# Optimization experiments

Hardware: AMD Instinct MI355X
Metric: run time of the kernel (lower is better)

The kernel has to match this reference:

```python
import jax, jax.numpy as jnp
import numpy as np

EPS = 1e-10

def setup_inputs() -> dict:
    key = jax.random.key(0)
    k0, k1, k2, k3, k4, k5 = jax.random.split(key, 6)
    B, S, V, C, D = 256, 20, 20000, 20, 64
    support_set_images = jax.random.uniform(k0, (B, S, V), dtype=jnp.float32)
    support_set_y_one_hot = jax.nn.one_hot(jax.random.randint(k1, (B, S), 0, C), C, dtype=jnp.float32)
    target_image = jax.random.uniform(k2, (B, V), dtype=jnp.float32)
    target_y = jax.random.randint(k3, (B,), 0, C)
    W = jax.random.normal(k4, (D, V), dtype=jnp.float32) * (1.0 / np.sqrt(V).astype(np.float32))
    b = jax.random.normal(k5, (D,), dtype=jnp.float32) * 0.01
    return dict(support_set_images=support_set_images,
                support_set_y_one_hot=support_set_y_one_hot,
                target_image=target_image, target_y=target_y, W=W, b=b)


def reference(support_set_images, support_set_y_one_hot, target_image, target_y, W, b):
    # SentenceEncoder (Linear vocab->64), applied to each support item and the target.
    sup = jnp.einsum('bsv,dv->bsd', support_set_images, W) + b        # [B,S,64]
    tgt = target_image @ W.T + b                                      # [B,64]

    # DistanceNetwork: dot(target, support) * rsqrt(clamp(||support||^2, eps))
    # (only the support vector's magnitude is normalized -- faithful to source).
    mag = jax.lax.rsqrt(jnp.clip(jnp.sum(sup * sup, axis=-1), EPS, None))  # [B,S]
    dots = jnp.einsum('bsd,bd->bs', sup, tgt)                              # [B,S]
    similarities = dots * mag                                              # [B,S]

    # AttentionalClassify: softmax over support, weighted combine of labels.
    attn = jax.nn.softmax(similarities, axis=-1)                           # [B,S]
    preds = jnp.einsum('bs,bsc->bc', attn, support_set_y_one_hot)          # [B,C]

    indices = jnp.argmax(preds, axis=1)
    accuracy = jnp.mean((indices == target_y).astype(jnp.float32))
    # F.cross_entropy applies log_softmax to preds (even though preds are already pdfs).
    logp = jax.nn.log_softmax(preds, axis=-1)
    crossentropy_loss = -jnp.mean(jnp.take_along_axis(logp, target_y[:, None], axis=1))
    return accuracy, crossentropy_loss
```

## Files before the change

kernel.cpp:

```cpp
#include <hip/hip_runtime.h>
#include <hip/hip_bf16.h>
#include <math.h>

#define B_  256
#define S_  20
#define V_  20000
#define C_  20
#define D_  64
#define MTOT (B_*S_ + B_)
#define KSPLIT 25
#define NK32 625
#define NKC  25

typedef __bf16 bf16x8 __attribute__((ext_vector_type(8)));
typedef float  f32x4  __attribute__((ext_vector_type(4)));

__device__ __forceinline__ void split8(const float4 a, const float4 b,
                                       uint4& hi, uint4& lo) {
    const float f[8] = {a.x, a.y, a.z, a.w, b.x, b.y, b.z, b.w};
    unsigned int h[8]; float r[8];
#pragma unroll
    for (int j = 0; j < 8; ++j) {
        const unsigned int u = __float_as_uint(f[j]);
        h[j] = u & 0xFFFF0000u;
        r[j] = f[j] - __uint_as_float(h[j]);
    }
    hi.x = (h[0] >> 16) | h[1];
    hi.y = (h[2] >> 16) | h[3];
    hi.z = (h[4] >> 16) | h[5];
    hi.w = (h[6] >> 16) | h[7];
    lo.x = (__float_as_uint(r[0]) >> 16) | (__float_as_uint(r[1]) & 0xFFFF0000u);
    lo.y = (__float_as_uint(r[2]) >> 16) | (__float_as_uint(r[3]) & 0xFFFF0000u);
    lo.z = (__float_as_uint(r[4]) >> 16) | (__float_as_uint(r[5]) & 0xFFFF0000u);
    lo.w = (__float_as_uint(r[6]) >> 16) | (__float_as_uint(r[7]) & 0xFFFF0000u);
}

__global__ __launch_bounds__(256)
void wconv_kernel(const float* __restrict__ W,
                  uint4* __restrict__ Wfh, uint4* __restrict__ Wfl) {
    const int g    = blockIdx.x * 256 + threadIdx.x;
    const int lane = g & 63;
    const int tt   = (g >> 6) & 3;
    const int c    = g >> 8;
    const int ln = lane & 15, qd = lane >> 4;
    const float* src = W + (size_t)(16 * tt + ln) * V_ + c * 32 + qd * 8;
    const float4 a = *(const float4*)src;
    const float4 b = *(const float4*)(src + 4);
    uint4 h, l; split8(a, b, h, l);
    Wfh[g] = h; Wfl[g] = l;
}

__global__ __launch_bounds__(256, 2)
void gemm3_kernel(const float* __restrict__ sup,
                  const float* __restrict__ tgtim,
                  const uint4* __restrict__ Wfh,
                  const uint4* __restrict__ Wfl,
                  float* __restrict__ Ep) {
    const int bmx = blockIdx.x;
    const int bk  = blockIdx.y;
    const int t = threadIdx.x;
    const int w = t >> 6, lane = t & 63;
    const int ln = lane & 15, qd = lane >> 4;
    const int mrow0 = bmx * 256 + w * 64;

    const float* xbase = (mrow0 < B_*S_)
        ? (sup   + (size_t)mrow0 * V_)
        : (tgtim + (size_t)(mrow0 - B_*S_) * V_);
    const float* xr0 = xbase + (size_t)ln * V_ + qd * 8;
    const float* xr1 = xr0 + (size_t)16 * V_;
    const float* xr2 = xr1 + (size_t)16 * V_;
    const float* xr3 = xr2 + (size_t)16 * V_;
    const uint4* wbh = Wfh + lane;
    const uint4* wbl = Wfl + lane;
    const int c0 = bk * NKC;

    f32x4 acc[4][4];
#pragma unroll
    for (int i = 0; i < 4; ++i)
#pragma unroll
        for (int j = 0; j < 4; ++j) acc[i][j] = (f32x4){0.f, 0.f, 0.f, 0.f};

    float4 aA[4][2], aB[4][2];
    uint4 whA[4], wlA[4], whB[4], wlB[4];

#define LDA(buf, c) do {                                                      \
    const size_t off_ = (size_t)(c) * 32;                                     \
    buf[0][0] = *(const float4*)(xr0 + off_);                                 \
    buf[0][1] = *(const float4*)(xr0 + off_ + 4);                             \
    buf[1][0] = *(const float4*)(xr1 + off_);                                 \
    buf[1][1] = *(const float4*)(xr1 + off_ + 4);                             \
    buf[2][0] = *(const float4*)(xr2 + off_);                                 \
    buf[2][1] = *(const float4*)(xr2 + off_ + 4);                             \
    buf[3][0] = *(const float4*)(xr3 + off_);                                 \
    buf[3][1] = *(const float4*)(xr3 + off_ + 4);                             \
} while (0)

#define LDW(bh_, bl_, c) do {                                                 \
    const uint4* ph_ = wbh + (size_t)(c) * 256;                               \
    const uint4* pl_ = wbl + (size_t)(c) * 256;                               \
    _Pragma("unroll")                                                         \
    for (int tt = 0; tt < 4; ++tt) { bh_[tt] = ph_[tt*64]; bl_[tt] = pl_[tt*64]; } \
} while (0)

#define STEP(abuf, bh_, bl_) do {                                             \
    _Pragma("unroll")                                                         \
    for (int af = 0; af < 4; ++af) {                                          \
        uint4 hu_, lu_; split8(abuf[af][0], abuf[af][1], hu_, lu_);           \
        const bf16x8 ah_ = *(const bf16x8*)&hu_;                              \
        const bf16x8 al_ = *(const bf16x8*)&lu_;                              \
        _Pragma("unroll")                                                     \
        for (int tt = 0; tt < 4; ++tt) {                                      \
            const bf16x8 bh2_ = *(const bf16x8*)&bh_[tt];                     \
            const bf16x8 bl2_ = *(const bf16x8*)&bl_[tt];                     \
            acc[af][tt] = __builtin_amdgcn_mfma_f32_16x16x32_bf16(ah_, bh2_, acc[af][tt], 0, 0, 0); \
            acc[af][tt] = __builtin_amdgcn_mfma_f32_16x16x32_bf16(ah_, bl2_, acc[af][tt], 0, 0, 0); \
            acc[af][tt] = __builtin_amdgcn_mfma_f32_16x16x32_bf16(al_, bh2_, acc[af][tt], 0, 0, 0); \
        }                                                                     \
    }                                                                         \
} while (0)

    LDA(aA, c0); LDW(whA, wlA, c0);
#pragma unroll 1
    for (int ii = 0; ii < (NKC - 1) / 2; ++ii) {
        const int c1 = c0 + 2 * ii + 1;
        LDA(aB, c1); LDW(whB, wlB, c1);
        STEP(aA, whA, wlA);
        const int c2 = c0 + 2 * ii + 2;
        LDA(aA, c2); LDW(whA, wlA, c2);
        STEP(aB, whB, wlB);
    }
    STEP(aA, whA, wlA);

#undef LDA
#undef LDW
#undef STEP

    float* dst = Ep + ((size_t)bk * MTOT + mrow0 + qd * 4) * D_ + ln;
#pragma unroll
    for (int af = 0; af < 4; ++af)
#pragma unroll
        for (int tt = 0; tt < 4; ++tt)
#pragma unroll
            for (int r = 0; r < 4; ++r)
                dst[(size_t)(af * 16 + r) * D_ + 16 * tt] = acc[af][tt][r];
}

__global__ __launch_bounds__(256)
void reduce_kernel(float* __restrict__ Ep) {
    const size_t i = (size_t)blockIdx.x * 256 + threadIdx.x;
    const size_t stride = (size_t)MTOT * D_;
    float4 s = *(const float4*)(Ep + i * 4);
#pragma unroll
    for (int p = 1; p < KSPLIT; ++p) {
        const float4 v = *(const float4*)(Ep + p * stride + i * 4);
        s.x += v.x; s.y += v.y; s.z += v.z; s.w += v.w;
    }
    *(float4*)(Ep + i * 4) = s;
}

__global__ __launch_bounds__(64)
void phase2_kernel(const float* __restrict__ E0,
                   const float* __restrict__ bias,
                   const float* __restrict__ onehot,
                   const int*   __restrict__ ty_,
                   float* __restrict__ res) {
    const int b = blockIdx.x;
    const int d = threadIdx.x;
    const float bv = bias[d];

    float supv[S_];
#pragma unroll
    for (int s = 0; s < S_; ++s)
        supv[s] = E0[((size_t)b * S_ + s) * D_ + d] + bv;
    float tg = E0[((size_t)(B_ * S_) + b) * D_ + d] + bv;

    float sims[S_];
#pragma unroll
    for (int s = 0; s < S_; ++s) {
        float q = supv[s] * supv[s];
        float r = supv[s] * tg;
#pragma unroll
        for (int off = 32; off; off >>= 1) {
            q += __shfl_xor(q, off);
            r += __shfl_xor(r, off);
        }
        sims[s] = r * rsqrtf(fmaxf(q, 1e-10f));
    }

    float mx = sims[0];
#pragma unroll
    for (int s = 1; s < S_; ++s) mx = fmaxf(mx, sims[s]);
    float se = 0.f;
#pragma unroll
    for (int s = 0; s < S_; ++s) { sims[s] = expf(sims[s] - mx); se += sims[s]; }
    const float inv = 1.f / se;

    float pc = -INFINITY;
    if (d < C_) {
        pc = 0.f;
#pragma unroll
        for (int s = 0; s < S_; ++s)
            pc += sims[s] * inv * onehot[((size_t)b * S_ + s) * C_ + d];
    }

    float v = pc;
    int idx = (d < C_) ? d : (1 << 30);
#pragma unroll
    for (int off = 32; off; off >>= 1) {
        const float ov = __shfl_xor(v, off);
        const int   oi = __shfl_xor(idx, off);
        if (ov > v || (ov == v && oi < idx)) { v = ov; idx = oi; }
    }
    float e = (d < C_) ? expf(pc - v) : 0.f;
#pragma unroll
    for (int off = 32; off; off >>= 1) e += __shfl_xor(e, off);
    const float lse = v + logf(e);

    const int ty = ty_[b];
    const float pty = __shfl(pc, ty);

    if (d == 0) {
        res[b]      = (idx == ty) ? 1.f : 0.f;
        res[B_ + b] = lse - pty;
    }
}

__global__ __launch_bounds__(64)
void phase3_kernel(const float* __restrict__ res, float* __restrict__ out) {
    const int t = threadIdx.x;
    float c = 0.f, l = 0.f;
#pragma unroll
    for (int i = 0; i < 4; ++i) {
        c += res[t + 64 * i];
        l += res[B_ + t + 64 * i];
    }
#pragma unroll
    for (int off = 32; off; off >>= 1) {
        c += __shfl_xor(c, off);
        l += __shfl_xor(l, off);
    }
    if (t == 0) {
        out[0] = c * (1.f / 256.f);
        out[1] = l * (1.f / 256.f);
    }
}

extern "C" void kernel_launch(void* const* d_in, const int* in_sizes, int n_in,
                              void* d_out, int out_size, void* d_ws, size_t ws_size,
                              hipStream_t stream) {
    const float* sup    = (const float*)d_in[0];
    const float* onehot = (const float*)d_in[1];
    const float* tgtim  = (const float*)d_in[2];
    const int*   ty     = (const int*)  d_in[3];
    const float* W      = (const float*)d_in[4];
    const float* bias   = (const float*)d_in[5];

    float* Ep  = (float*)d_ws;
    float* res = Ep + (size_t)KSPLIT * MTOT * D_;
    uint4* Wfh = (uint4*)(res + 512);
    uint4* Wfl = Wfh + (size_t)NK32 * 4 * 64;
    float* out = (float*)d_out;

    wconv_kernel<<<625, 256, 0, stream>>>(W, Wfh, Wfl);
    gemm3_kernel<<<dim3(21, KSPLIT), 256, 0, stream>>>(sup, tgtim, Wfh, Wfl, Ep);
    reduce_kernel<<<(MTOT * D_ / 4) / 256, 256, 0, stream>>>(Ep);
    phase2_kernel<<<B_, 64, 0, stream>>>(Ep, bias, onehot, ty, res);
    phase3_kernel<<<1, 64, 0, stream>>>(res, out);
}
```

Measured before the change: 647.8 us.

## Halve GEMM split-K count and fuse reduction, classify and mean kernels

```diff
diff --git a/kernel.cpp b/kernel.cpp
--- a/kernel.cpp
+++ b/kernel.cpp
@@ -8,9 +8,9 @@
 #define C_  20
 #define D_  64
 #define MTOT (B_*S_ + B_)
-#define KSPLIT 25
+#define KSPLIT 12
+#define KCH 52
 #define NK32 625
-#define NKC  25
 
 typedef __bf16 bf16x8 __attribute__((ext_vector_type(8)));
 typedef float  f32x4  __attribute__((ext_vector_type(4)));
@@ -37,7 +37,9 @@
 
 __global__ __launch_bounds__(256)
 void wconv_kernel(const float* __restrict__ W,
-                  uint4* __restrict__ Wfh, uint4* __restrict__ Wfl) {
+                  uint4* __restrict__ Wfh, uint4* __restrict__ Wfl,
+                  unsigned* __restrict__ ctr) {
+    if (blockIdx.x == 0 && threadIdx.x == 0) *ctr = 0u;
     const int g    = blockIdx.x * 256 + threadIdx.x;
     const int lane = g & 63;
     const int tt   = (g >> 6) & 3;
@@ -72,7 +74,9 @@
     const float* xr3 = xr2 + (size_t)16 * V_;
     const uint4* wbh = Wfh + lane;
     const uint4* wbl = Wfl + lane;
-    const int c0 = bk * NKC;
+
+    const int c0 = bk * KCH;
+    const int nk = (bk == KSPLIT - 1) ? (NK32 - KCH * (KSPLIT - 1)) : KCH;
 
     f32x4 acc[4][4];
 #pragma unroll
@@ -120,16 +124,17 @@
 } while (0)
 
     LDA(aA, c0); LDW(whA, wlA, c0);
+    int i = 0;
 #pragma unroll 1
-    for (int ii = 0; ii < (NKC - 1) / 2; ++ii) {
-        const int c1 = c0 + 2 * ii + 1;
+    for (; i + 2 <= nk; i += 2) {
+        const int c1 = c0 + i + 1;
         LDA(aB, c1); LDW(whB, wlB, c1);
         STEP(aA, whA, wlA);
-        const int c2 = c0 + 2 * ii + 2;
+        const int c2 = c0 + ((i + 2 < nk) ? (i + 2) : (i + 1));
         LDA(aA, c2); LDW(whA, wlA, c2);
         STEP(aB, whB, wlB);
     }
-    STEP(aA, whA, wlA);
+    if (i < nk) STEP(aA, whA, wlA);
 
 #undef LDA
 #undef LDW
@@ -146,102 +151,117 @@
 }
 
 __global__ __launch_bounds__(256)
-void reduce_kernel(float* __restrict__ Ep) {
-    const size_t i = (size_t)blockIdx.x * 256 + threadIdx.x;
+void phase23_kernel(const float* __restrict__ Ep,
+                    const float* __restrict__ bias,
+                    const float* __restrict__ onehot,
+                    const int*   __restrict__ ty_,
+                    float* __restrict__ res,
+                    unsigned* __restrict__ ctr,
+                    float* __restrict__ out) {
+    const int b = blockIdx.x;
+    const int t = threadIdx.x;
+    __shared__ float sm[21 * 64];
     const size_t stride = (size_t)MTOT * D_;
-    float4 s = *(const float4*)(Ep + i * 4);
-#pragma unroll
-    for (int p = 1; p < KSPLIT; ++p) {
-        const float4 v = *(const float4*)(Ep + p * stride + i * 4);
-        s.x += v.x; s.y += v.y; s.z += v.z; s.w += v.w;
-    }
-    *(float4*)(Ep + i * 4) = s;
-}
-
-__global__ __launch_bounds__(64)
-void phase2_kernel(const float* __restrict__ E0,
-                   const float* __restrict__ bias,
-                   const float* __restrict__ onehot,
-                   const int*   __restrict__ ty_,
-                   float* __restrict__ res) {
-    const int b = blockIdx.x;
-    const int d = threadIdx.x;
-    const float bv = bias[d];
-
-    float supv[S_];
-#pragma unroll
-    for (int s = 0; s < S_; ++s)
-        supv[s] = E0[((size_t)b * S_ + s) * D_ + d] + bv;
-    float tg = E0[((size_t)(B_ * S_) + b) * D_ + d] + bv;
-
-    float sims[S_];
-#pragma unroll
-    for (int s = 0; s < S_; ++s) {
-        float q = supv[s] * supv[s];
-        float r = supv[s] * tg;
+
+#pragma unroll
+    for (int base = 0; base < 21 * 64; base += 256) {
+        const int idx = base + t;
+        if (idx < 21 * 64) {
+            const int row = idx >> 6, d = idx & 63;
+            const size_t grow = (row < S_) ? ((size_t)b * S_ + row)
+                                           : ((size_t)(B_ * S_) + b);
+            const float* p0 = Ep + grow * D_ + d;
+            float s = 0.f;
+#pragma unroll
+            for (int p = 0; p < KSPLIT; ++p) s += p0[(size_t)p * stride];
+            sm[idx] = s;
+        }
+    }
+    __syncthreads();
+
+    if (t < 64) {
+        const int d = t;
+        const float bv = bias[d];
+
+        float supv[S_];
+#pragma unroll
+        for (int s = 0; s < S_; ++s) supv[s] = sm[s * 64 + d] + bv;
+        float tg = sm[S_ * 64 + d] + bv;
+
+        float sims[S_];
+#pragma unroll
+        for (int s = 0; s < S_; ++s) {
+            float q = supv[s] * supv[s];
+            float r = supv[s] * tg;
+#pragma unroll
+            for (int off = 32; off; off >>= 1) {
+                q += __shfl_xor(q, off);
+                r += __shfl_xor(r, off);
+            }
+            sims[s] = r * rsqrtf(fmaxf(q, 1e-10f));
+        }
+
+        float mx = sims[0];
+#pragma unroll
+        for (int s = 1; s < S_; ++s) mx = fmaxf(mx, sims[s]);
+        float se = 0.f;
+#pragma unroll
+        for (int s = 0; s < S_; ++s) { sims[s] = expf(sims[s] - mx); se += sims[s]; }
+        const float inv = 1.f / se;
+
+        float pc = -INFINITY;
+        if (d < C_) {
+            pc = 0.f;
+#pragma unroll
+            for (int s = 0; s < S_; ++s)
+                pc += sims[s] * inv * onehot[((size_t)b * S_ + s) * C_ + d];
+        }
+
+        float v = pc;
+        int idx = (d < C_) ? d : (1 << 30);
 #pragma unroll
         for (int off = 32; off; off >>= 1) {
-            q += __shfl_xor(q, off);
-            r += __shfl_xor(r, off);
-        }
-        sims[s] = r * rsqrtf(fmaxf(q, 1e-10f));
-    }
-
-    float mx = sims[0];
-#pragma unroll
-    for (int s = 1; s < S_; ++s) mx = fmaxf(mx, sims[s]);
-    float se = 0.f;
-#pragma unroll
-    for (int s = 0; s < S_; ++s) { sims[s] = expf(sims[s] - mx); se += sims[s]; }
-    const float inv = 1.f / se;
-
-    float pc = -INFINITY;
-    if (d < C_) {
-        pc = 0.f;
-#pragma unroll
-        for (int s = 0; s < S_; ++s)
-            pc += sims[s] * inv * onehot[((size_t)b * S_ + s) * C_ + d];
-    }
-
-    float v = pc;
-    int idx = (d < C_) ? d : (1 << 30);
-#pragma unroll
-    for (int off = 32; off; off >>= 1) {
-        const float ov = __shfl_xor(v, off);
-        const int   oi = __shfl_xor(idx, off);
-        if (ov > v || (ov == v && oi < idx)) { v = ov; idx = oi; }
-    }
-    float e = (d < C_) ? expf(pc - v) : 0.f;
-#pragma unroll
-    for (int off = 32; off; off >>= 1) e += __shfl_xor(e, off);
-    const float lse = v + logf(e);
-
-    const int ty = ty_[b];
-    const float pty = __shfl(pc, ty);
-
-    if (d == 0) {
-        res[b]      = (idx == ty) ? 1.f : 0.f;
-        res[B_ + b] = lse - pty;
-    }
-}
-
-__global__ __launch_bounds__(64)
-void phase3_kernel(const float* __restrict__ res, float* __restrict__ out) {
-    const int t = threadIdx.x;
-    float c = 0.f, l = 0.f;
-#pragma unroll
-    for (int i = 0; i < 4; ++i) {
-        c += res[t + 64 * i];
-        l += res[B_ + t + 64 * i];
-    }
-#pragma unroll
-    for (int off = 32; off; off >>= 1) {
-        c += __shfl_xor(c, off);
-        l += __shfl_xor(l, off);
-    }
-    if (t == 0) {
-        out[0] = c * (1.f / 256.f);
-        out[1] = l * (1.f / 256.f);
+            const float ov = __shfl_xor(v, off);
+            const int   oi = __shfl_xor(idx, off);
+            if (ov > v || (ov == v && oi < idx)) { v = ov; idx = oi; }
+        }
+        float e = (d < C_) ? expf(pc - v) : 0.f;
+#pragma unroll
+        for (int off = 32; off; off >>= 1) e += __shfl_xor(e, off);
+        const float lse = v + logf(e);
+
+        const int ty = ty_[b];
+        const float pty = __shfl(pc, ty);
+
+        if (d == 0) {
+            res[b]      = (idx == ty) ? 1.f : 0.f;
+            res[B_ + b] = lse - pty;
+        }
+    }
+
+    __threadfence();
+    __shared__ unsigned lastv;
+    if (t == 0) lastv = atomicAdd(ctr, 1u);
+    __syncthreads();
+    if (lastv == (unsigned)(B_ - 1)) {
+        __threadfence();
+        if (t < 64) {
+            float c = 0.f, l = 0.f;
+#pragma unroll
+            for (int i = 0; i < 4; ++i) {
+                c += res[t + 64 * i];
+                l += res[B_ + t + 64 * i];
+            }
+#pragma unroll
+            for (int off = 32; off; off >>= 1) {
+                c += __shfl_xor(c, off);
+                l += __shfl_xor(l, off);
+            }
+            if (t == 0) {
+                out[0] = c * (1.f / 256.f);
+                out[1] = l * (1.f / 256.f);
+            }
+        }
     }
 }
 
@@ -257,13 +277,12 @@
 
     float* Ep  = (float*)d_ws;
     float* res = Ep + (size_t)KSPLIT * MTOT * D_;
-    uint4* Wfh = (uint4*)(res + 512);
+    unsigned* ctr = (unsigned*)(res + 512);
+    uint4* Wfh = (uint4*)(res + 512 + 4);
     uint4* Wfl = Wfh + (size_t)NK32 * 4 * 64;
     float* out = (float*)d_out;
 
-    wconv_kernel<<<625, 256, 0, stream>>>(W, Wfh, Wfl);
+    wconv_kernel<<<625, 256, 0, stream>>>(W, Wfh, Wfl, ctr);
     gemm3_kernel<<<dim3(21, KSPLIT), 256, 0, stream>>>(sup, tgtim, Wfh, Wfl, Ep);
-    reduce_kernel<<<(MTOT * D_ / 4) / 256, 256, 0, stream>>>(Ep);
-    phase2_kernel<<<B_, 64, 0, stream>>>(Ep, bias, onehot, ty, res);
-    phase3_kernel<<<1, 64, 0, stream>>>(res, out);
-}
+    phase23_kernel<<<B_, 256, 0, stream>>>(Ep, bias, onehot, ty, res, ctr, out);
+}
```

Measured after the change: 617.0 us, median of 2. 1.05x faster.
